# Kernel optimization log

Hardware: AMD Instinct MI355X
Metric: run time of the kernel (lower is better)

## Reference

```python
import jax, jax.numpy as jnp
import numpy as np

N_NODES = 50000
N_EDGES = 800000
IN_F = 256
OUT_F = 128
ALPHA = 0.2  # LeakyReLU negative slope


def setup_inputs() -> dict:
    key = jax.random.key(0)
    k_h, k_row, k_col, k_W, k_a = jax.random.split(key, 5)
    h = jax.random.normal(k_h, (N_NODES, IN_F), dtype=jnp.float32)
    row = jax.random.randint(k_row, (N_EDGES,), 0, N_NODES)
    # Guarantee every node appears as a destination so unique(dst) == arange(N)
    col = jnp.concatenate([
        jnp.arange(N_NODES),
        jax.random.randint(k_col, (N_EDGES - N_NODES,), 0, N_NODES),
    ])
    adj = jnp.stack([row, col]).astype(jnp.int64)
    # Xavier-uniform-ish params (gain 1.414)
    lim_W = 1.414 * np.sqrt(6.0 / (IN_F + OUT_F))
    W = jax.random.uniform(k_W, (IN_F, OUT_F), minval=-lim_W, maxval=lim_W, dtype=jnp.float32)
    lim_a = 1.414 * np.sqrt(6.0 / (2 * OUT_F + 1))
    a = jax.random.uniform(k_a, (2 * OUT_F, 1), minval=-lim_a, maxval=lim_a, dtype=jnp.float32)
    return {"h": h, "adj": adj, "W": W, "a": a}


def reference(h, adj, W, a):
    N = h.shape[0]
    self_loops = jnp.arange(N)  # == unique(adj[1]) by input construction
    row = jnp.concatenate([adj[0], self_loops])  # [E_total]
    col = jnp.concatenate([adj[1], self_loops])  # [E_total]

    Wh = h @ W                                    # [N, OUT_F]
    s_src = (Wh @ a[:OUT_F]).squeeze(-1)          # [N] (Wh1)
    s_dst = (Wh @ a[OUT_F:]).squeeze(-1)          # [N] (Wh2)

    e = jax.nn.leaky_relu(s_dst[col] + s_src[row], negative_slope=ALPHA)  # [E_total]

    # segment softmax over destination nodes
    e_max = jax.ops.segment_max(e, col, num_segments=N)
    ex = jnp.exp(e - e_max[col])
    denom = jax.ops.segment_sum(ex, col, num_segments=N)
    att = ex / denom[col]                         # [E_total]

    h_prime = jax.ops.segment_sum(Wh[row] * att[:, None], col, num_segments=N)  # [N, OUT_F]
    return jax.nn.elu(h_prime)  # concat=True
```

## Files before the change

kernel.cpp:

```cpp
#include <hip/hip_runtime.h>
#include <math.h>

#define N_NODES 50000
#define N_EDGES 800000
#define IN_F 256
#define OUT_F 128
#define ALPHA 0.2f

#define B_DST 32
#define B_EDGE 16
#define R_NODES 1563
#define CHUNK_E (N_EDGES / B_EDGE)
#define CAP_C 12
#define RAW_STRIDE (B_EDGE * CAP_C)
#define SCAT_BLOCKS (B_DST * B_EDGE)
#define SLOT_CAP 64

#define COMPACT_BLOCKS ((N_NODES + 255) / 256)
#define GEMM_WAVES (2 * ((N_NODES + 15) / 16))
#define GEMM_BLOCKS ((GEMM_WAVES + 3) / 4)

typedef short bf16x8 __attribute__((ext_vector_type(8)));
typedef float f32x4  __attribute__((ext_vector_type(4)));

static __device__ __forceinline__ unsigned short f2bf(float f) {
    unsigned int u = __float_as_uint(f);
    u += 0x7FFFu + ((u >> 16) & 1u);
    return (unsigned short)(u >> 16);
}
static __device__ __forceinline__ float bf2f(unsigned int u16) {
    return __uint_as_float(u16 << 16);
}

__global__ __launch_bounds__(256, 4) void k_prep(const float* __restrict__ W,
                                                 const float* __restrict__ a,
                                                 const int* __restrict__ adj,
                                                 float* __restrict__ Wa,
                                                 unsigned short* __restrict__ WbT,
                                                 unsigned short* __restrict__ slots_raw,
                                                 unsigned char* __restrict__ cnt8) {
    const int b = blockIdx.x, t = threadIdx.x;
    if (b < SCAT_BLOCKS) {
        const int j  = b % B_EDGE;
        const int di = b / B_EDGE;
        const int base = di * R_NODES;
        const int lim  = min(base + R_NODES, N_NODES);
        __shared__ int cl[R_NODES];
        for (int k = t; k < R_NODES; k += 256) cl[k] = 0;
        __syncthreads();
        const int e0 = j * CHUNK_E;
        const int4* dp = (const int4*)(adj + N_EDGES + e0);
        const int4* sp = (const int4*)(adj + e0);
        const int nit = CHUNK_E / 4;
        for (int it0 = t; it0 < nit; it0 += 1024) {
            int4 dv[4], sv[4];
#pragma unroll
            for (int u = 0; u < 4; ++u) {
                const int it = it0 + u * 256;
                if (it < nit) { dv[u] = dp[it]; sv[u] = sp[it]; }
                else          { dv[u] = make_int4(-1, -1, -1, -1); sv[u] = make_int4(0, 0, 0, 0); }
            }
#pragma unroll
            for (int u = 0; u < 4; ++u) {
                const int4 d = dv[u], s = sv[u];
                if (d.x >= base && d.x < lim) {
                    const int p = atomicAdd(&cl[d.x - base], 1);
                    if (p < CAP_C) slots_raw[(size_t)d.x * RAW_STRIDE + j * CAP_C + p] = (unsigned short)s.x;
                }
                if (d.y >= base && d.y < lim) {
                    const int p = atomicAdd(&cl[d.y - base], 1);
                    if (p < CAP_C) slots_raw[(size_t)d.y * RAW_STRIDE + j * CAP_C + p] = (unsigned short)s.y;
                }
                if (d.z >= base && d.z < lim) {
                    const int p = atomicAdd(&cl[d.z - base], 1);
                    if (p < CAP_C) slots_raw[(size_t)d.z * RAW_STRIDE + j * CAP_C + p] = (unsigned short)s.z;
                }
                if (d.w >= base && d.w < lim) {
                    const int p = atomicAdd(&cl[d.w - base], 1);
                    if (p < CAP_C) slots_raw[(size_t)d.w * RAW_STRIDE + j * CAP_C + p] = (unsigned short)s.w;
                }
            }
        }
        __syncthreads();
        for (int k = t; k < lim - base; k += 256)
            cnt8[(size_t)(base + k) * B_EDGE + j] = (unsigned char)min(cl[k], CAP_C);
    } else if (b == SCAT_BLOCKS) {
        const int k = t;
        const float4* wr  = (const float4*)(W + (size_t)k * OUT_F);
        const float4* av1 = (const float4*)a;
        const float4* av2 = (const float4*)(a + OUT_F);
        float s1 = 0.0f, s2 = 0.0f;
#pragma unroll 8
        for (int i = 0; i < OUT_F / 4; ++i) {
            float4 w = wr[i], x = av1[i], y = av2[i];
            s1 = fmaf(w.x, x.x, fmaf(w.y, x.y, fmaf(w.z, x.z, fmaf(w.w, x.w, s1))));
            s2 = fmaf(w.x, y.x, fmaf(w.y, y.y, fmaf(w.z, y.z, fmaf(w.w, y.w, s2))));
        }
        Wa[k] = s1;
        Wa[IN_F + k] = s2;
    } else {
        const int n = b - (SCAT_BLOCKS + 1);
        WbT[(size_t)n * IN_F + t] = f2bf(W[(size_t)t * OUT_F + n]);
    }
}

__global__ __launch_bounds__(256, 4) void k_gemm(const float* __restrict__ h,
                                                 const unsigned short* __restrict__ WbT,
                                                 const float* __restrict__ Wa,
                                                 unsigned short* __restrict__ Whb,
                                                 float* __restrict__ s_src,
                                                 float* __restrict__ s_dst,
                                                 unsigned short* __restrict__ slots_raw,
                                                 const unsigned char* __restrict__ cnt8,
                                                 int* __restrict__ cntT) {
    const int b = blockIdx.x;
    if (b < COMPACT_BLOCKS) {
        const int node = b * 256 + threadIdx.x;
        if (node >= N_NODES) return;
        const unsigned char* c8 = cnt8 + (size_t)node * B_EDGE;
        unsigned short* row = slots_raw + (size_t)node * RAW_STRIDE;
        int total = 0;
#pragma unroll
        for (int c = 0; c < B_EDGE; ++c) {
            const int dc = c8[c];
            const unsigned short* s = row + c * CAP_C;
            for (int k = 0; k < dc; ++k) {
                const unsigned short v = s[k];
                if (total < SLOT_CAP) row[total++] = v;
            }
        }
        cntT[node] = total;
        return;
    }
    const int gid = b - COMPACT_BLOCKS;
    const int wid = gid * 4 + (threadIdx.x >> 6);
    if (wid >= GEMM_WAVES) return;
    const int lane = threadIdx.x & 63;
    const int m = lane & 15, grp = lane >> 4;
    const int row  = (wid >> 1) * 16 + m;
    const int half = wid & 1;
    const unsigned short* wbase = WbT + (size_t)(half * 64 + m) * IN_F + grp * 8;
    const float* hrow = h + (size_t)row * IN_F + grp * 8;

    float4 hx[16];
#pragma unroll
    for (int kt = 0; kt < 8; ++kt) {
        hx[2 * kt]     = *(const float4*)(hrow + kt * 32);
        hx[2 * kt + 1] = *(const float4*)(hrow + kt * 32 + 4);
    }

    if (half == 0) {
        float sp1 = 0.0f, sp2 = 0.0f;
#pragma unroll
        for (int kt = 0; kt < 8; ++kt) {
            const float4 x0 = hx[2 * kt], x1 = hx[2 * kt + 1];
            const float4* wap1 = (const float4*)(Wa + kt * 32 + grp * 8);
            const float4* wap2 = (const float4*)(Wa + IN_F + kt * 32 + grp * 8);
            float4 a0 = wap1[0], a1 = wap1[1];
            float4 b0 = wap2[0], b1 = wap2[1];
            sp1 = fmaf(x0.x, a0.x, fmaf(x0.y, a0.y, fmaf(x0.z, a0.z, fmaf(x0.w, a0.w, sp1))));
            sp1 = fmaf(x1.x, a1.x, fmaf(x1.y, a1.y, fmaf(x1.z, a1.z, fmaf(x1.w, a1.w, sp1))));
            sp2 = fmaf(x0.x, b0.x, fmaf(x0.y, b0.y, fmaf(x0.z, b0.z, fmaf(x0.w, b0.w, sp2))));
            sp2 = fmaf(x1.x, b1.x, fmaf(x1.y, b1.y, fmaf(x1.z, b1.z, fmaf(x1.w, b1.w, sp2))));
        }
        float t1 = sp1, t2 = sp2;
        t1 += __shfl_xor(t1, 16); t1 += __shfl_xor(t1, 32);
        t2 += __shfl_xor(t2, 16); t2 += __shfl_xor(t2, 32);
        if (grp == 0) { s_src[row] = t1; s_dst[row] = t2; }
    }

    bf16x8 hf[8];
#pragma unroll
    for (int kt = 0; kt < 8; ++kt) {
        const float4 x0 = hx[2 * kt], x1 = hx[2 * kt + 1];
        bf16x8 f;
        f[0] = (short)f2bf(x0.x); f[1] = (short)f2bf(x0.y);
        f[2] = (short)f2bf(x0.z); f[3] = (short)f2bf(x0.w);
        f[4] = (short)f2bf(x1.x); f[5] = (short)f2bf(x1.y);
        f[6] = (short)f2bf(x1.z); f[7] = (short)f2bf(x1.w);
        hf[kt] = f;
    }

    f32x4 acc[4];
#pragma unroll
    for (int nt = 0; nt < 4; ++nt) acc[nt] = (f32x4){0.f, 0.f, 0.f, 0.f};
#pragma unroll
    for (int kt = 0; kt < 8; ++kt) {
#pragma unroll
        for (int nt = 0; nt < 4; ++nt) {
            bf16x8 wf = *(const bf16x8*)(wbase + (size_t)nt * 16 * IN_F + kt * 32);
            acc[nt] = __builtin_amdgcn_mfma_f32_16x16x32_bf16(wf, hf[kt], acc[nt], 0, 0, 0);
        }
    }

    unsigned short* orow = Whb + (size_t)row * OUT_F + half * 64;
#pragma unroll
    for (int nt = 0; nt < 4; ++nt) {
        f32x4 v = acc[nt];
        ushort4 pk;
        pk.x = f2bf(v[0]); pk.y = f2bf(v[1]);
        pk.z = f2bf(v[2]); pk.w = f2bf(v[3]);
        *(ushort4*)(orow + nt * 16 + grp * 4) = pk;
    }
}

__global__ __launch_bounds__(256, 4) void k_gather(const unsigned short* __restrict__ Whb,
                                                   const int* __restrict__ cntT,
                                                   const unsigned short* __restrict__ slots_raw,
                                                   const float* __restrict__ s_src,
                                                   const float* __restrict__ s_dst,
                                                   float* __restrict__ out) {
    const int wid  = (blockIdx.x * blockDim.x + threadIdx.x) >> 6;
    const int lane = threadIdx.x & 63;
    const int grp  = lane >> 4;
    const int l    = lane & 15;
    const int node = wid * 4 + grp;
    if (node >= N_NODES) return;

    const float sd = s_dst[node];
    float s0 = sd + s_src[node];
    float lr0 = (s0 > 0.0f) ? s0 : ALPHA * s0;
    float x0 = __expf(lr0);
    uint4 w0 = ((const uint4*)(Whb + (size_t)node * OUT_F))[l];
    float a0 = x0 * bf2f(w0.x & 0xFFFFu);
    float a1 = x0 * bf2f(w0.x >> 16);
    float a2 = x0 * bf2f(w0.y & 0xFFFFu);
    float a3 = x0 * bf2f(w0.y >> 16);
    float a4 = x0 * bf2f(w0.z & 0xFFFFu);
    float a5 = x0 * bf2f(w0.z >> 16);
    float a6 = x0 * bf2f(w0.w & 0xFFFFu);
    float a7 = x0 * bf2f(w0.w >> 16);
    float dsum = x0;

    const int deg = min(cntT[node], SLOT_CAP);
    const unsigned short* __restrict__ srow = slots_raw + (size_t)node * RAW_STRIDE;

    for (int i = 0; i < deg; i += 8) {
        const uint4 q = *(const uint4*)(srow + i);
        unsigned su[8];
        su[0] = q.x & 0xFFFFu; su[1] = q.x >> 16;
        su[2] = q.y & 0xFFFFu; su[3] = q.y >> 16;
        su[4] = q.z & 0xFFFFu; su[5] = q.z >> 16;
        su[6] = q.w & 0xFFFFu; su[7] = q.w >> 16;
#pragma unroll
        for (int j = 0; j < 8; ++j)
            su[j] = (i + j < deg) ? min(su[j], N_NODES - 1u) : (unsigned)node;
        float e[8];
#pragma unroll
        for (int j = 0; j < 8; ++j) e[j] = sd + s_src[su[j]];
        uint4 v[8];
#pragma unroll
        for (int j = 0; j < 8; ++j) v[j] = ((const uint4*)(Whb + (size_t)su[j] * OUT_F))[l];
        float x[8];
#pragma unroll
        for (int j = 0; j < 8; ++j) {
            float lr = (e[j] > 0.0f) ? e[j] : ALPHA * e[j];
            float xv = __expf(lr);
            x[j] = (i + j < deg) ? xv : 0.0f;
        }
#pragma unroll
        for (int j = 0; j < 8; ++j) dsum += x[j];
#pragma unroll
        for (int j = 0; j < 8; ++j) {
            a0 = fmaf(x[j], bf2f(v[j].x & 0xFFFFu), a0);
            a1 = fmaf(x[j], bf2f(v[j].x >> 16), a1);
            a2 = fmaf(x[j], bf2f(v[j].y & 0xFFFFu), a2);
            a3 = fmaf(x[j], bf2f(v[j].y >> 16), a3);
            a4 = fmaf(x[j], bf2f(v[j].z & 0xFFFFu), a4);
            a5 = fmaf(x[j], bf2f(v[j].z >> 16), a5);
            a6 = fmaf(x[j], bf2f(v[j].w & 0xFFFFu), a6);
            a7 = fmaf(x[j], bf2f(v[j].w >> 16), a7);
        }
    }

    const float inv = 1.0f / dsum;
    float4 o0, o1;
    o0.x = a0 * inv; o0.y = a1 * inv; o0.z = a2 * inv; o0.w = a3 * inv;
    o1.x = a4 * inv; o1.y = a5 * inv; o1.z = a6 * inv; o1.w = a7 * inv;
    o0.x = (o0.x > 0.0f) ? o0.x : expm1f(o0.x);
    o0.y = (o0.y > 0.0f) ? o0.y : expm1f(o0.y);
    o0.z = (o0.z > 0.0f) ? o0.z : expm1f(o0.z);
    o0.w = (o0.w > 0.0f) ? o0.w : expm1f(o0.w);
    o1.x = (o1.x > 0.0f) ? o1.x : expm1f(o1.x);
    o1.y = (o1.y > 0.0f) ? o1.y : expm1f(o1.y);
    o1.z = (o1.z > 0.0f) ? o1.z : expm1f(o1.z);
    o1.w = (o1.w > 0.0f) ? o1.w : expm1f(o1.w);
    float4* op = (float4*)(out + (size_t)node * OUT_F + l * 8);
    op[0] = o0;
    op[1] = o1;
}

extern "C" void kernel_launch(void* const* d_in, const int* in_sizes, int n_in,
                              void* d_out, int out_size, void* d_ws, size_t ws_size,
                              hipStream_t stream) {
    const float* h   = (const float*)d_in[0];
    const int*   adj = (const int*)d_in[1];
    const float* W   = (const float*)d_in[2];
    const float* a   = (const float*)d_in[3];
    float* out = (float*)d_out;

    char* ws = (char*)d_ws;
    const size_t SZ_WHB  = (size_t)N_NODES * OUT_F * 2;
    const size_t SZ_N    = 200704;
    const size_t SZ_C8   = 802816;
    unsigned short* Whb   = (unsigned short*)(ws);
    float* s_src          = (float*)(ws + SZ_WHB);
    float* s_dst          = (float*)(ws + SZ_WHB + SZ_N);
    int*   cntT           = (int*)  (ws + SZ_WHB + 2 * SZ_N);
    float* Wa             = (float*)(ws + SZ_WHB + 3 * SZ_N);
    unsigned short* WbT   = (unsigned short*)(ws + SZ_WHB + 3 * SZ_N + 2048);
    unsigned char* cnt8   = (unsigned char*)(ws + SZ_WHB + 3 * SZ_N + 2048 + 65536);
    unsigned short* slots_raw = (unsigned short*)(ws + SZ_WHB + 3 * SZ_N + 2048 + 65536 + SZ_C8);

    (void)in_sizes; (void)n_in; (void)out_size; (void)ws_size;

    k_prep  <<<SCAT_BLOCKS + 1 + OUT_F, 256, 0, stream>>>(W, a, adj, Wa, WbT,
                                                          slots_raw, cnt8);
    k_gemm  <<<COMPACT_BLOCKS + GEMM_BLOCKS, 256, 0, stream>>>(h, WbT, Wa, Whb,
                                                               s_src, s_dst,
                                                               slots_raw, cnt8,
                                                               cntT);
    k_gather<<<(N_NODES / 4 * 64) / 256, 256, 0, stream>>>(Whb, cntT, slots_raw,
                                                           s_src, s_dst, out);
}
```

Measured before the change: 201.2 us.

## Pre-convert h to bf16, compute full 128-col tile per wave, derive scores from Wh

```diff
diff --git a/kernel.cpp b/kernel.cpp
--- a/kernel.cpp
+++ b/kernel.cpp
@@ -16,8 +16,9 @@
 #define SCAT_BLOCKS (B_DST * B_EDGE)
 #define SLOT_CAP 64
 
+#define CONV_BLOCKS (N_NODES * IN_F / 8 / 256)
 #define COMPACT_BLOCKS ((N_NODES + 255) / 256)
-#define GEMM_WAVES (2 * ((N_NODES + 15) / 16))
+#define GEMM_WAVES ((N_NODES + 15) / 16)
 #define GEMM_BLOCKS ((GEMM_WAVES + 3) / 4)
 
 typedef short bf16x8 __attribute__((ext_vector_type(8)));
@@ -32,81 +33,78 @@
     return __uint_as_float(u16 << 16);
 }
 
-__global__ __launch_bounds__(256, 4) void k_prep(const float* __restrict__ W,
-                                                 const float* __restrict__ a,
-                                                 const int* __restrict__ adj,
-                                                 float* __restrict__ Wa,
-                                                 unsigned short* __restrict__ WbT,
+__global__ __launch_bounds__(256, 4) void k_scat(const int* __restrict__ adj,
                                                  unsigned short* __restrict__ slots_raw,
                                                  unsigned char* __restrict__ cnt8) {
     const int b = blockIdx.x, t = threadIdx.x;
-    if (b < SCAT_BLOCKS) {
-        const int j  = b % B_EDGE;
-        const int di = b / B_EDGE;
-        const int base = di * R_NODES;
-        const int lim  = min(base + R_NODES, N_NODES);
-        __shared__ int cl[R_NODES];
-        for (int k = t; k < R_NODES; k += 256) cl[k] = 0;
-        __syncthreads();
-        const int e0 = j * CHUNK_E;
-        const int4* dp = (const int4*)(adj + N_EDGES + e0);
-        const int4* sp = (const int4*)(adj + e0);
-        const int nit = CHUNK_E / 4;
-        for (int it0 = t; it0 < nit; it0 += 1024) {
-            int4 dv[4], sv[4];
-#pragma unroll
-            for (int u = 0; u < 4; ++u) {
-                const int it = it0 + u * 256;
-                if (it < nit) { dv[u] = dp[it]; sv[u] = sp[it]; }
-                else          { dv[u] = make_int4(-1, -1, -1, -1); sv[u] = make_int4(0, 0, 0, 0); }
-            }
-#pragma unroll
-            for (int u = 0; u < 4; ++u) {
-                const int4 d = dv[u], s = sv[u];
-                if (d.x >= base && d.x < lim) {
-                    const int p = atomicAdd(&cl[d.x - base], 1);
-                    if (p < CAP_C) slots_raw[(size_t)d.x * RAW_STRIDE + j * CAP_C + p] = (unsigned short)s.x;
-                }
-                if (d.y >= base && d.y < lim) {
-                    const int p = atomicAdd(&cl[d.y - base], 1);
-                    if (p < CAP_C) slots_raw[(size_t)d.y * RAW_STRIDE + j * CAP_C + p] = (unsigned short)s.y;
-                }
-                if (d.z >= base && d.z < lim) {
-                    const int p = atomicAdd(&cl[d.z - base], 1);
-                    if (p < CAP_C) slots_raw[(size_t)d.z * RAW_STRIDE + j * CAP_C + p] = (unsigned short)s.z;
-                }
-                if (d.w >= base && d.w < lim) {
-                    const int p = atomicAdd(&cl[d.w - base], 1);
-                    if (p < CAP_C) slots_raw[(size_t)d.w * RAW_STRIDE + j * CAP_C + p] = (unsigned short)s.w;
-                }
-            }
-        }
-        __syncthreads();
-        for (int k = t; k < lim - base; k += 256)
-            cnt8[(size_t)(base + k) * B_EDGE + j] = (unsigned char)min(cl[k], CAP_C);
-    } else if (b == SCAT_BLOCKS) {
-        const int k = t;
-        const float4* wr  = (const float4*)(W + (size_t)k * OUT_F);
-        const float4* av1 = (const float4*)a;
-        const float4* av2 = (const float4*)(a + OUT_F);
-        float s1 = 0.0f, s2 = 0.0f;
-#pragma unroll 8
-        for (int i = 0; i < OUT_F / 4; ++i) {
-            float4 w = wr[i], x = av1[i], y = av2[i];
-            s1 = fmaf(w.x, x.x, fmaf(w.y, x.y, fmaf(w.z, x.z, fmaf(w.w, x.w, s1))));
-            s2 = fmaf(w.x, y.x, fmaf(w.y, y.y, fmaf(w.z, y.z, fmaf(w.w, y.w, s2))));
-        }
-        Wa[k] = s1;
-        Wa[IN_F + k] = s2;
-    } else {
-        const int n = b - (SCAT_BLOCKS + 1);
-        WbT[(size_t)n * IN_F + t] = f2bf(W[(size_t)t * OUT_F + n]);
-    }
-}
-
-__global__ __launch_bounds__(256, 4) void k_gemm(const float* __restrict__ h,
+    const int j  = b % B_EDGE;
+    const int di = b / B_EDGE;
+    const int base = di * R_NODES;
+    const int lim  = min(base + R_NODES, N_NODES);
+    __shared__ int cl[R_NODES];
+    for (int k = t; k < R_NODES; k += 256) cl[k] = 0;
+    __syncthreads();
+    const int e0 = j * CHUNK_E;
+    const int4* dp = (const int4*)(adj + N_EDGES + e0);
+    const int4* sp = (const int4*)(adj + e0);
+    const int nit = CHUNK_E / 4;
+    for (int it0 = t; it0 < nit; it0 += 1024) {
+        int4 dv[4], sv[4];
+#pragma unroll
+        for (int u = 0; u < 4; ++u) {
+            const int it = it0 + u * 256;
+            if (it < nit) { dv[u] = dp[it]; sv[u] = sp[it]; }
+            else          { dv[u] = make_int4(-1, -1, -1, -1); sv[u] = make_int4(0, 0, 0, 0); }
+        }
+#pragma unroll
+        for (int u = 0; u < 4; ++u) {
+            const int4 d = dv[u], s = sv[u];
+            if (d.x >= base && d.x < lim) {
+                const int p = atomicAdd(&cl[d.x - base], 1);
+                if (p < CAP_C) slots_raw[(size_t)d.x * RAW_STRIDE + j * CAP_C + p] = (unsigned short)s.x;
+            }
+            if (d.y >= base && d.y < lim) {
+                const int p = atomicAdd(&cl[d.y - base], 1);
+                if (p < CAP_C) slots_raw[(size_t)d.y * RAW_STRIDE + j * CAP_C + p] = (unsigned short)s.y;
+            }
+            if (d.z >= base && d.z < lim) {
+                const int p = atomicAdd(&cl[d.z - base], 1);
+                if (p < CAP_C) slots_raw[(size_t)d.z * RAW_STRIDE + j * CAP_C + p] = (unsigned short)s.z;
+            }
+            if (d.w >= base && d.w < lim) {
+                const int p = atomicAdd(&cl[d.w - base], 1);
+                if (p < CAP_C) slots_raw[(size_t)d.w * RAW_STRIDE + j * CAP_C + p] = (unsigned short)s.w;
+            }
+        }
+    }
+    __syncthreads();
+    for (int k = t; k < lim - base; k += 256)
+        cnt8[(size_t)(base + k) * B_EDGE + j] = (unsigned char)min(cl[k], CAP_C);
+}
+
+__global__ __launch_bounds__(256) void k_prep2(const float* __restrict__ W,
+                                               const float* __restrict__ h,
+                                               unsigned short* __restrict__ WbT,
+                                               unsigned short* __restrict__ hb) {
+    const int b = blockIdx.x, t = threadIdx.x;
+    if (b < OUT_F) {
+        WbT[(size_t)b * IN_F + t] = f2bf(W[(size_t)t * OUT_F + b]);
+        return;
+    }
+    const size_t base = ((size_t)(b - OUT_F) * 256 + t) * 8;
+    const float4* hp = (const float4*)(h + base);
+    const float4 x0 = hp[0], x1 = hp[1];
+    bf16x8 v;
+    v[0] = (short)f2bf(x0.x); v[1] = (short)f2bf(x0.y);
+    v[2] = (short)f2bf(x0.z); v[3] = (short)f2bf(x0.w);
+    v[4] = (short)f2bf(x1.x); v[5] = (short)f2bf(x1.y);
+    v[6] = (short)f2bf(x1.z); v[7] = (short)f2bf(x1.w);
+    *(bf16x8*)(hb + base) = v;
+}
+
+__global__ __launch_bounds__(256, 4) void k_gemm(const unsigned short* __restrict__ hb,
                                                  const unsigned short* __restrict__ WbT,
-                                                 const float* __restrict__ Wa,
+                                                 const float* __restrict__ a,
                                                  unsigned short* __restrict__ Whb,
                                                  float* __restrict__ s_src,
                                                  float* __restrict__ s_dst,
@@ -137,65 +135,42 @@
     if (wid >= GEMM_WAVES) return;
     const int lane = threadIdx.x & 63;
     const int m = lane & 15, grp = lane >> 4;
-    const int row  = (wid >> 1) * 16 + m;
-    const int half = wid & 1;
-    const unsigned short* wbase = WbT + (size_t)(half * 64 + m) * IN_F + grp * 8;
-    const float* hrow = h + (size_t)row * IN_F + grp * 8;
-
-    float4 hx[16];
+    const int row = wid * 16 + m;
+    const unsigned short* hrow = hb + (size_t)row * IN_F + grp * 8;
+    const unsigned short* wbase = WbT + (size_t)m * IN_F + grp * 8;
+
+    bf16x8 hf[8];
+#pragma unroll
+    for (int kt = 0; kt < 8; ++kt) hf[kt] = *(const bf16x8*)(hrow + kt * 32);
+
+    f32x4 acc[8];
+#pragma unroll
+    for (int nt = 0; nt < 8; ++nt) acc[nt] = (f32x4){0.f, 0.f, 0.f, 0.f};
 #pragma unroll
     for (int kt = 0; kt < 8; ++kt) {
-        hx[2 * kt]     = *(const float4*)(hrow + kt * 32);
-        hx[2 * kt + 1] = *(const float4*)(hrow + kt * 32 + 4);
-    }
-
-    if (half == 0) {
-        float sp1 = 0.0f, sp2 = 0.0f;
-#pragma unroll
-        for (int kt = 0; kt < 8; ++kt) {
-            const float4 x0 = hx[2 * kt], x1 = hx[2 * kt + 1];
-            const float4* wap1 = (const float4*)(Wa + kt * 32 + grp * 8);
-            const float4* wap2 = (const float4*)(Wa + IN_F + kt * 32 + grp * 8);
-            float4 a0 = wap1[0], a1 = wap1[1];
-            float4 b0 = wap2[0], b1 = wap2[1];
-            sp1 = fmaf(x0.x, a0.x, fmaf(x0.y, a0.y, fmaf(x0.z, a0.z, fmaf(x0.w, a0.w, sp1))));
-            sp1 = fmaf(x1.x, a1.x, fmaf(x1.y, a1.y, fmaf(x1.z, a1.z, fmaf(x1.w, a1.w, sp1))));
-            sp2 = fmaf(x0.x, b0.x, fmaf(x0.y, b0.y, fmaf(x0.z, b0.z, fmaf(x0.w, b0.w, sp2))));
-            sp2 = fmaf(x1.x, b1.x, fmaf(x1.y, b1.y, fmaf(x1.z, b1.z, fmaf(x1.w, b1.w, sp2))));
-        }
-        float t1 = sp1, t2 = sp2;
-        t1 += __shfl_xor(t1, 16); t1 += __shfl_xor(t1, 32);
-        t2 += __shfl_xor(t2, 16); t2 += __shfl_xor(t2, 32);
-        if (grp == 0) { s_src[row] = t1; s_dst[row] = t2; }
-    }
-
-    bf16x8 hf[8];
-#pragma unroll
-    for (int kt = 0; kt < 8; ++kt) {
-        const float4 x0 = hx[2 * kt], x1 = hx[2 * kt + 1];
-        bf16x8 f;
-        f[0] = (short)f2bf(x0.x); f[1] = (short)f2bf(x0.y);
-        f[2] = (short)f2bf(x0.z); f[3] = (short)f2bf(x0.w);
-        f[4] = (short)f2bf(x1.x); f[5] = (short)f2bf(x1.y);
-        f[6] = (short)f2bf(x1.z); f[7] = (short)f2bf(x1.w);
-        hf[kt] = f;
-    }
-
-    f32x4 acc[4];
-#pragma unroll
-    for (int nt = 0; nt < 4; ++nt) acc[nt] = (f32x4){0.f, 0.f, 0.f, 0.f};
-#pragma unroll
-    for (int kt = 0; kt < 8; ++kt) {
-#pragma unroll
-        for (int nt = 0; nt < 4; ++nt) {
+#pragma unroll
+        for (int nt = 0; nt < 8; ++nt) {
             bf16x8 wf = *(const bf16x8*)(wbase + (size_t)nt * 16 * IN_F + kt * 32);
             acc[nt] = __builtin_amdgcn_mfma_f32_16x16x32_bf16(wf, hf[kt], acc[nt], 0, 0, 0);
         }
     }
 
-    unsigned short* orow = Whb + (size_t)row * OUT_F + half * 64;
-#pragma unroll
-    for (int nt = 0; nt < 4; ++nt) {
+    float s1 = 0.0f, s2 = 0.0f;
+#pragma unroll
+    for (int nt = 0; nt < 8; ++nt) {
+        const float4 a1 = *(const float4*)(a + nt * 16 + grp * 4);
+        const float4 a2 = *(const float4*)(a + OUT_F + nt * 16 + grp * 4);
+        const f32x4 v = acc[nt];
+        s1 = fmaf(v[0], a1.x, fmaf(v[1], a1.y, fmaf(v[2], a1.z, fmaf(v[3], a1.w, s1))));
+        s2 = fmaf(v[0], a2.x, fmaf(v[1], a2.y, fmaf(v[2], a2.z, fmaf(v[3], a2.w, s2))));
+    }
+    s1 += __shfl_xor(s1, 16); s1 += __shfl_xor(s1, 32);
+    s2 += __shfl_xor(s2, 16); s2 += __shfl_xor(s2, 32);
+    if (grp == 0) { s_src[row] = s1; s_dst[row] = s2; }
+
+    unsigned short* orow = Whb + (size_t)row * OUT_F;
+#pragma unroll
+    for (int nt = 0; nt < 8; ++nt) {
         f32x4 v = acc[nt];
         ushort4 pk;
         pk.x = f2bf(v[0]); pk.y = f2bf(v[1]);
@@ -303,23 +278,23 @@
     const size_t SZ_WHB  = (size_t)N_NODES * OUT_F * 2;
     const size_t SZ_N    = 200704;
     const size_t SZ_C8   = 802816;
+    const size_t SZ_RAW  = (size_t)N_NODES * RAW_STRIDE * 2;
     unsigned short* Whb   = (unsigned short*)(ws);
     float* s_src          = (float*)(ws + SZ_WHB);
     float* s_dst          = (float*)(ws + SZ_WHB + SZ_N);
     int*   cntT           = (int*)  (ws + SZ_WHB + 2 * SZ_N);
-    float* Wa             = (float*)(ws + SZ_WHB + 3 * SZ_N);
-    unsigned short* WbT   = (unsigned short*)(ws + SZ_WHB + 3 * SZ_N + 2048);
-    unsigned char* cnt8   = (unsigned char*)(ws + SZ_WHB + 3 * SZ_N + 2048 + 65536);
-    unsigned short* slots_raw = (unsigned short*)(ws + SZ_WHB + 3 * SZ_N + 2048 + 65536 + SZ_C8);
+    unsigned short* WbT   = (unsigned short*)(ws + SZ_WHB + 3 * SZ_N);
+    unsigned char* cnt8   = (unsigned char*)(ws + SZ_WHB + 3 * SZ_N + 65536);
+    unsigned short* slots_raw = (unsigned short*)(ws + SZ_WHB + 3 * SZ_N + 65536 + SZ_C8);
+    unsigned short* hb    = (unsigned short*)(ws + SZ_WHB + 3 * SZ_N + 65536 + SZ_C8 + SZ_RAW);
 
     (void)in_sizes; (void)n_in; (void)out_size; (void)ws_size;
 
-    k_prep  <<<SCAT_BLOCKS + 1 + OUT_F, 256, 0, stream>>>(W, a, adj, Wa, WbT,
-                                                          slots_raw, cnt8);
-    k_gemm  <<<COMPACT_BLOCKS + GEMM_BLOCKS, 256, 0, stream>>>(h, WbT, Wa, Whb,
+    k_scat  <<<SCAT_BLOCKS, 256, 0, stream>>>(adj, slots_raw, cnt8);
+    k_prep2 <<<OUT_F + CONV_BLOCKS, 256, 0, stream>>>(W, h, WbT, hb);
+    k_gemm  <<<COMPACT_BLOCKS + GEMM_BLOCKS, 256, 0, stream>>>(hb, WbT, a, Whb,
                                                                s_src, s_dst,
-                                                               slots_raw, cnt8,
-                                                               cntT);
+                                                               slots_raw, cnt8, cntT);
     k_gather<<<(N_NODES / 4 * 64) / 256, 256, 0, stream>>>(Whb, cntT, slots_raw,
                                                            s_src, s_dst, out);
 }
```

New measurement: 208.4 us. +3.6%, slower.
